# Kernel tuning notes

Hardware: AMD Instinct MI355X
Metric: run time of the kernel (lower is better)

## Reference

```python
import jax, jax.numpy as jnp
import numpy as np

B, T, ENC_H, DEC_H, ATTN = 128, 2048, 512, 512, 128


def setup_inputs() -> dict:
    key = jax.random.key(0)
    k1, k2, k3, k4, k5 = jax.random.split(key, 5)
    s = lambda fan_in: 1.0 / np.sqrt(fan_in)
    return {
        "encoder_outputs": jax.random.normal(k1, (B, T, ENC_H), dtype=jnp.float32),
        "decoder_hidden": jax.random.normal(k2, (B, DEC_H), dtype=jnp.float32),
        # nn.Linear weights are [out_features, in_features]
        "W_enc": jax.random.uniform(k3, (ATTN, ENC_H), jnp.float32, -s(ENC_H), s(ENC_H)),
        "W_dec": jax.random.uniform(k4, (ATTN, DEC_H), jnp.float32, -s(DEC_H), s(DEC_H)),
        "v_w": jax.random.uniform(k5, (1, ATTN), jnp.float32, -s(ATTN), s(ATTN)),
    }


def reference(encoder_outputs, decoder_hidden, W_enc, W_dec, v_w):
    # enc_proj: [B, T, A]
    enc_proj = jnp.einsum("bth,ah->bta", encoder_outputs, W_enc)
    # dec_proj: [B, 1, A]
    dec_proj = jnp.einsum("bh,ah->ba", decoder_hidden, W_dec)[:, None, :]
    energy = jnp.tanh(enc_proj + dec_proj)                      # [B, T, A]
    scores = jnp.einsum("bta,a->bt", energy, v_w[0])            # [B, T]
    weights = jax.nn.softmax(scores, axis=-1)                   # [B, T]
    context = jnp.einsum("bt,bth->bh", weights, encoder_outputs)  # [B, ENC_H]
    return context, weights
```

## Files before the change

### kernel.cpp

```cpp
#include <hip/hip_runtime.h>
#include <hip/hip_bf16.h>

#define B_SZ   128
#define T_SZ   2048
#define ENCH   512
#define ATTN_  128
#define NBLK   256
#define STRIPS_PER_BLK 8

typedef __attribute__((ext_vector_type(8))) short short8;
typedef __attribute__((ext_vector_type(4))) float f32x4;

__device__ __forceinline__ unsigned short f2bf_rne(float f) {
  unsigned u = __builtin_bit_cast(unsigned, f);
  u += 0x7FFFu + ((u >> 16) & 1u);
  return (unsigned short)(u >> 16);
}
__device__ __forceinline__ float fast_tanh(float x) {
  float e = __expf(2.f * x);
  return 1.f - __fdividef(2.f, e + 1.f);
}
__device__ __forceinline__ short8 pack8(float4 a, float4 b) {
  union { unsigned u[4]; short8 s; } r;
  asm("v_cvt_pk_bf16_f32 %0, %1, %2" : "=v"(r.u[0]) : "v"(a.x), "v"(a.y));
  asm("v_cvt_pk_bf16_f32 %0, %1, %2" : "=v"(r.u[1]) : "v"(a.z), "v"(a.w));
  asm("v_cvt_pk_bf16_f32 %0, %1, %2" : "=v"(r.u[2]) : "v"(b.x), "v"(b.y));
  asm("v_cvt_pk_bf16_f32 %0, %1, %2" : "=v"(r.u[3]) : "v"(b.z), "v"(b.w));
  return r.s;
}
template<int CTRL>
__device__ __forceinline__ float dpp_add(float v) {
  int t = __builtin_amdgcn_update_dpp(0, __builtin_bit_cast(int, v),
                                      CTRL, 0xf, 0xf, true);
  return v + __builtin_bit_cast(float, t);
}
__device__ __forceinline__ float sum16(float v) {
  v = dpp_add<0xB1>(v);
  v = dpp_add<0x4E>(v);
  v = dpp_add<0x141>(v);
  v = dpp_add<0x140>(v);
  return v;
}

__global__ void k_prep(const float* __restrict__ w,
                       unsigned short* __restrict__ o,
                       const float* __restrict__ dec,
                       const float* __restrict__ wdec,
                       float* __restrict__ dout) {
  if (blockIdx.x < 32) {
    int idx = blockIdx.x * 256 + threadIdx.x;
    int l   = idx & 63;
    int wks = idx >> 6;
    int cg  = wks >> 4, ks = wks & 15;
    int row = cg * 16 + (l & 15);
    int col = ks * 32 + (l >> 4) * 8;
    const float4* src = reinterpret_cast<const float4*>(w + row * ENCH + col);
    float4 v0 = src[0], v1 = src[1];
    short8 r;
    r[0] = (short)f2bf_rne(v0.x); r[1] = (short)f2bf_rne(v0.y);
    r[2] = (short)f2bf_rne(v0.z); r[3] = (short)f2bf_rne(v0.w);
    r[4] = (short)f2bf_rne(v1.x); r[5] = (short)f2bf_rne(v1.y);
    r[6] = (short)f2bf_rne(v1.z); r[7] = (short)f2bf_rne(v1.w);
    *reinterpret_cast<short8*>(o + (size_t)idx * 8) = r;
  } else {
    __shared__ float dh[ENCH];
    int b = blockIdx.x - 32, tid = threadIdx.x;
    for (int i = tid; i < ENCH; i += 256) dh[i] = dec[b * ENCH + i];
    __syncthreads();
    if (tid < 128) {
      const float4* wr4 = reinterpret_cast<const float4*>(wdec + tid * ENCH);
      float acc = 0.f;
      for (int h4 = 0; h4 < ENCH / 4; ++h4) {
        float4 w4 = wr4[h4];
        acc += dh[h4 * 4 + 0] * w4.x + dh[h4 * 4 + 1] * w4.y +
               dh[h4 * 4 + 2] * w4.z + dh[h4 * 4 + 3] * w4.w;
      }
      dout[b * ATTN_ + tid] = acc;
    }
  }
}

__global__ __launch_bounds__(512, 2) void k_main(
    const float* __restrict__ enc,
    const unsigned short* __restrict__ wfrag,
    const float* __restrict__ decproj,
    const float* __restrict__ vw,
    float* __restrict__ scores_raw,
    float* __restrict__ ctx_part,
    float* __restrict__ ml_part)
{
  const int tid  = threadIdx.x;
  const int lane = tid & 63;
  const int wid  = tid >> 6;
  const int l15  = lane & 15;
  const int g    = lane >> 4;

  __shared__ unsigned short w_lds[ATTN_ * ENCH];

#pragma unroll
  for (int r = 0; r < 16; ++r) {
    int i = r * 512 + tid;
    reinterpret_cast<short8*>(w_lds)[i] = reinterpret_cast<const short8*>(wfrag)[i];
  }

  const int b       = blockIdx.x >> 1;
  const int s16base = (blockIdx.x & 1) * 8;
  float vv[8], dv[8];
#pragma unroll
  for (int cg = 0; cg < 8; ++cg) {
    vv[cg] = vw[cg * 16 + l15];
    dv[cg] = decproj[b * ATTN_ + cg * 16 + l15];
  }
  __syncthreads();

#pragma unroll 1
  for (int k = 0; k < wid; ++k) __builtin_amdgcn_s_sleep(12);

#pragma unroll 1
  for (int i = 0; i < STRIPS_PER_BLK; ++i) {
    const int s16  = s16base + i;
    const int row0 = s16 * 128 + wid * 16;
    const float* arow = enc + ((size_t)b * T_SZ + row0 + l15) * ENCH + g * 8;

    float4 r0[16], r1[16];
#pragma unroll
    for (int ks = 0; ks < 16; ++ks) {
      r0[ks] = *reinterpret_cast<const float4*>(arow + ks * 32);
      r1[ks] = *reinterpret_cast<const float4*>(arow + ks * 32 + 4);
    }

    f32x4 acc[8];
#pragma unroll
    for (int cg = 0; cg < 8; ++cg) acc[cg] = (f32x4){0.f, 0.f, 0.f, 0.f};
#pragma unroll
    for (int ks = 0; ks < 16; ++ks) {
      short8 af = pack8(r0[ks], r1[ks]);
      const char* wb = (const char*)w_lds + ks * 1024 + lane * 16;
#pragma unroll
      for (int cg = 0; cg < 8; ++cg) {
        short8 bf = *reinterpret_cast<const short8*>(wb + cg * 16384);
        acc[cg] = __builtin_amdgcn_mfma_f32_16x16x32_bf16(af, bf, acc[cg], 0, 0, 0);
      }
    }

    float er[4];
#pragma unroll
    for (int r = 0; r < 4; ++r) {
      float e = 0.f;
#pragma unroll
      for (int cg = 0; cg < 8; ++cg)
        e += fast_tanh(acc[cg][r] + dv[cg]) * vv[cg];
      er[r] = sum16(e);
    }
    if (l15 == 0) {
#pragma unroll
      for (int r = 0; r < 4; ++r)
        scores_raw[(size_t)b * T_SZ + row0 + g * 4 + r] = er[r];
    }

    float mg = fmaxf(fmaxf(er[0], er[1]), fmaxf(er[2], er[3]));
    mg = fmaxf(mg, __shfl_xor(mg, 16));
    mg = fmaxf(mg, __shfl_xor(mg, 32));
    float x0 = __expf(er[0] - mg), x1 = __expf(er[1] - mg);
    float x2 = __expf(er[2] - mg), x3 = __expf(er[3] - mg);
    float xs = (x0 + x1) + (x2 + x3);
    xs += __shfl_xor(xs, 16);
    xs += __shfl_xor(xs, 32);
    const float l_run = xs;
    float sel = (l15 & 3) == 0 ? er[0]
              : (l15 & 3) == 1 ? er[1]
              : (l15 & 3) == 2 ? er[2] : er[3];
    float smine = __shfl(sel, ((l15 >> 2) << 4) | (l15 & 3));
    const float p_me = __expf(smine - mg);

    float ctx8[8];
#pragma unroll
    for (int j = 0; j < 8; ++j) ctx8[j] = 0.f;
#pragma unroll
    for (int ks = 0; ks < 16; ++ks) {
      float c[8];
      c[0] = p_me * r0[ks].x; c[1] = p_me * r0[ks].y;
      c[2] = p_me * r0[ks].z; c[3] = p_me * r0[ks].w;
      c[4] = p_me * r1[ks].x; c[5] = p_me * r1[ks].y;
      c[6] = p_me * r1[ks].z; c[7] = p_me * r1[ks].w;
#pragma unroll
      for (int j = 0; j < 8; ++j) c[j] = sum16(c[j]);
      if (l15 == ks) {
#pragma unroll
        for (int j = 0; j < 8; ++j) ctx8[j] = c[j];
      }
    }

    const size_t widx = (size_t)b * 128 + s16 * 8 + wid;
    float* cp = ctx_part + widx * ENCH + l15 * 32 + g * 8;
    *reinterpret_cast<float4*>(cp)     = (float4){ctx8[0], ctx8[1], ctx8[2], ctx8[3]};
    *reinterpret_cast<float4*>(cp + 4) = (float4){ctx8[4], ctx8[5], ctx8[6], ctx8[7]};
    if (lane == 0) {
      ml_part[widx * 2 + 0] = mg;
      ml_part[widx * 2 + 1] = l_run;
    }
  }
}

__global__ void k_combine(const float* __restrict__ ctx_part,
                          const float* __restrict__ ml_part,
                          float* __restrict__ out_ctx,
                          float* __restrict__ weights)
{
  __shared__ float msh[128], lsh[128], fac[128];
  int b = blockIdx.x, tid = threadIdx.x;
  if (tid < 128) {
    msh[tid] = ml_part[((size_t)b * 128 + tid) * 2 + 0];
    lsh[tid] = ml_part[((size_t)b * 128 + tid) * 2 + 1];
  }
  __syncthreads();
  float M = msh[0];
  for (int w = 1; w < 128; ++w) M = fmaxf(M, msh[w]);
  if (tid < 128) fac[tid] = __expf(msh[tid] - M);
  __syncthreads();
  float L = 0.f;
  for (int w = 0; w < 128; ++w) L += fac[w] * lsh[w];
  float Linv = 1.f / L;
  for (int h = tid; h < ENCH; h += 256) {
    float a = 0.f;
    for (int w = 0; w < 128; ++w)
      a += fac[w] * ctx_part[((size_t)b * 128 + w) * ENCH + h];
    out_ctx[b * ENCH + h] = a * Linv;
  }
  for (int t = tid; t < T_SZ; t += 256) {
    float raw = weights[(size_t)b * T_SZ + t];
    weights[(size_t)b * T_SZ + t] = __expf(raw - M) * Linv;
  }
}

extern "C" void kernel_launch(void* const* d_in, const int* in_sizes, int n_in,
                              void* d_out, int out_size, void* d_ws, size_t ws_size,
                              hipStream_t stream) {
  const float* enc  = (const float*)d_in[0];
  const float* dec  = (const float*)d_in[1];
  const float* wenc = (const float*)d_in[2];
  const float* wdec = (const float*)d_in[3];
  const float* vw   = (const float*)d_in[4];

  float* out     = (float*)d_out;
  float* out_ctx = out;
  float* out_w   = out + B_SZ * ENCH;

  char* ws = (char*)d_ws;
  unsigned short* wfrag = (unsigned short*)ws;
  float* decproj  = (float*)(ws + 131072);
  float* ml_part  = (float*)(ws + 131072 + 65536);
  float* ctx_part = (float*)(ws + 131072 + 65536 + 131072);

  hipLaunchKernelGGL(k_prep, dim3(160), dim3(256), 0, stream,
                     wenc, wfrag, dec, wdec, decproj);
  hipLaunchKernelGGL(k_main, dim3(NBLK), dim3(512), 0, stream,
                     enc, wfrag, decproj, vw, out_w, ctx_part, ml_part);
  hipLaunchKernelGGL(k_combine, dim3(B_SZ), dim3(256), 0, stream,
                     ctx_part, ml_part, out_ctx, out_w);
}
```

Measured before the change: 173.2 us.

## Double waves per block by keeping encoder tiles as bf16 and splitting accumulators

The main kernel now launches 1024-thread blocks, each covering four 256-row segments, instead of 512-thread blocks covering eight 128-row strips. Each wave keeps its encoder tile only as packed bf16 MFMA fragments rather than fp32 copies. The projection is done in two halves of four column groups with fewer live accumulators, and the decoder projection and v vectors move to LDS. This cuts register use so twice as many waves per CU can hide global load latency in this bandwidth-bound kernel. The trade-off is that the context sum now uses bf16-rounded encoder values, which lowers its precision.

```diff
diff --git a/kernel.cpp b/kernel.cpp
--- a/kernel.cpp
+++ b/kernel.cpp
@@ -6,7 +6,7 @@
 #define ENCH   512
 #define ATTN_  128
 #define NBLK   256
-#define STRIPS_PER_BLK 8
+#define SEGS_PER_BLK 4
 
 typedef __attribute__((ext_vector_type(8))) short short8;
 typedef __attribute__((ext_vector_type(4))) float f32x4;
@@ -40,6 +40,10 @@
   v = dpp_add<0x141>(v);
   v = dpp_add<0x140>(v);
   return v;
+}
+__device__ __forceinline__ float bfel(short8 v, int j_half, bool hi) {
+  unsigned u = __builtin_bit_cast(unsigned, (int)((((int*)&v))[j_half]));
+  return __builtin_bit_cast(float, hi ? (u & 0xFFFF0000u) : (u << 16));
 }
 
 __global__ void k_prep(const float* __restrict__ w,
@@ -80,7 +84,7 @@
   }
 }
 
-__global__ __launch_bounds__(512, 2) void k_main(
+__global__ __launch_bounds__(1024, 4) void k_main(
     const float* __restrict__ enc,
     const unsigned short* __restrict__ wfrag,
     const float* __restrict__ decproj,
@@ -96,62 +100,65 @@
   const int g    = lane >> 4;
 
   __shared__ unsigned short w_lds[ATTN_ * ENCH];
-
-#pragma unroll
-  for (int r = 0; r < 16; ++r) {
-    int i = r * 512 + tid;
+  __shared__ float dv_lds[ATTN_], vv_lds[ATTN_];
+
+  const int b    = blockIdx.x >> 1;
+  const int seg0 = (blockIdx.x & 1) * 4;
+
+#pragma unroll
+  for (int r = 0; r < 8; ++r) {
+    int i = r * 1024 + tid;
     reinterpret_cast<short8*>(w_lds)[i] = reinterpret_cast<const short8*>(wfrag)[i];
   }
-
-  const int b       = blockIdx.x >> 1;
-  const int s16base = (blockIdx.x & 1) * 8;
-  float vv[8], dv[8];
-#pragma unroll
-  for (int cg = 0; cg < 8; ++cg) {
-    vv[cg] = vw[cg * 16 + l15];
-    dv[cg] = decproj[b * ATTN_ + cg * 16 + l15];
-  }
+  if (tid < 128)       dv_lds[tid] = decproj[b * ATTN_ + tid];
+  else if (tid < 256)  vv_lds[tid - 128] = vw[tid - 128];
   __syncthreads();
 
 #pragma unroll 1
-  for (int k = 0; k < wid; ++k) __builtin_amdgcn_s_sleep(12);
+  for (int k = 0; k < wid; ++k) __builtin_amdgcn_s_sleep(6);
 
 #pragma unroll 1
-  for (int i = 0; i < STRIPS_PER_BLK; ++i) {
-    const int s16  = s16base + i;
-    const int row0 = s16 * 128 + wid * 16;
+  for (int i = 0; i < SEGS_PER_BLK; ++i) {
+    const int seg  = seg0 + i;
+    const int row0 = seg * 256 + wid * 16;
     const float* arow = enc + ((size_t)b * T_SZ + row0 + l15) * ENCH + g * 8;
 
-    float4 r0[16], r1[16];
+    short8 af[16];
 #pragma unroll
     for (int ks = 0; ks < 16; ++ks) {
-      r0[ks] = *reinterpret_cast<const float4*>(arow + ks * 32);
-      r1[ks] = *reinterpret_cast<const float4*>(arow + ks * 32 + 4);
-    }
-
-    f32x4 acc[8];
-#pragma unroll
-    for (int cg = 0; cg < 8; ++cg) acc[cg] = (f32x4){0.f, 0.f, 0.f, 0.f};
-#pragma unroll
-    for (int ks = 0; ks < 16; ++ks) {
-      short8 af = pack8(r0[ks], r1[ks]);
-      const char* wb = (const char*)w_lds + ks * 1024 + lane * 16;
-#pragma unroll
-      for (int cg = 0; cg < 8; ++cg) {
-        short8 bf = *reinterpret_cast<const short8*>(wb + cg * 16384);
-        acc[cg] = __builtin_amdgcn_mfma_f32_16x16x32_bf16(af, bf, acc[cg], 0, 0, 0);
+      float4 a0 = *reinterpret_cast<const float4*>(arow + ks * 32);
+      float4 a1 = *reinterpret_cast<const float4*>(arow + ks * 32 + 4);
+      af[ks] = pack8(a0, a1);
+    }
+
+    float e[4] = {0.f, 0.f, 0.f, 0.f};
+#pragma unroll 1
+    for (int half = 0; half < 2; ++half) {
+      f32x4 acc[4];
+#pragma unroll
+      for (int c = 0; c < 4; ++c) acc[c] = (f32x4){0.f, 0.f, 0.f, 0.f};
+#pragma unroll
+      for (int ks = 0; ks < 16; ++ks) {
+        const char* wb = (const char*)w_lds + ks * 1024 + lane * 16 + half * 65536;
+#pragma unroll
+        for (int c = 0; c < 4; ++c) {
+          short8 bf = *reinterpret_cast<const short8*>(wb + c * 16384);
+          acc[c] = __builtin_amdgcn_mfma_f32_16x16x32_bf16(af[ks], bf, acc[c], 0, 0, 0);
+        }
+      }
+#pragma unroll
+      for (int c = 0; c < 4; ++c) {
+        int col = (half * 4 + c) * 16 + l15;
+        float d = dv_lds[col], v = vv_lds[col];
+#pragma unroll
+        for (int r = 0; r < 4; ++r)
+          e[r] += fast_tanh(acc[c][r] + d) * v;
       }
     }
 
     float er[4];
 #pragma unroll
-    for (int r = 0; r < 4; ++r) {
-      float e = 0.f;
-#pragma unroll
-      for (int cg = 0; cg < 8; ++cg)
-        e += fast_tanh(acc[cg][r] + dv[cg]) * vv[cg];
-      er[r] = sum16(e);
-    }
+    for (int r = 0; r < 4; ++r) er[r] = sum16(e[r]);
     if (l15 == 0) {
 #pragma unroll
       for (int r = 0; r < 4; ++r)
@@ -179,10 +186,11 @@
 #pragma unroll
     for (int ks = 0; ks < 16; ++ks) {
       float c[8];
-      c[0] = p_me * r0[ks].x; c[1] = p_me * r0[ks].y;
-      c[2] = p_me * r0[ks].z; c[3] = p_me * r0[ks].w;
-      c[4] = p_me * r1[ks].x; c[5] = p_me * r1[ks].y;
-      c[6] = p_me * r1[ks].z; c[7] = p_me * r1[ks].w;
+#pragma unroll
+      for (int jh = 0; jh < 4; ++jh) {
+        c[jh * 2 + 0] = p_me * bfel(af[ks], jh, false);
+        c[jh * 2 + 1] = p_me * bfel(af[ks], jh, true);
+      }
 #pragma unroll
       for (int j = 0; j < 8; ++j) c[j] = sum16(c[j]);
       if (l15 == ks) {
@@ -191,7 +199,7 @@
       }
     }
 
-    const size_t widx = (size_t)b * 128 + s16 * 8 + wid;
+    const size_t widx = (size_t)b * 128 + seg * 16 + wid;
     float* cp = ctx_part + widx * ENCH + l15 * 32 + g * 8;
     *reinterpret_cast<float4*>(cp)     = (float4){ctx8[0], ctx8[1], ctx8[2], ctx8[3]};
     *reinterpret_cast<float4*>(cp + 4) = (float4){ctx8[4], ctx8[5], ctx8[6], ctx8[7]};
@@ -254,7 +262,7 @@
 
   hipLaunchKernelGGL(k_prep, dim3(160), dim3(256), 0, stream,
                      wenc, wfrag, dec, wdec, decproj);
-  hipLaunchKernelGGL(k_main, dim3(NBLK), dim3(512), 0, stream,
+  hipLaunchKernelGGL(k_main, dim3(NBLK), dim3(1024), 0, stream,
                      enc, wfrag, decproj, vw, out_w, ctx_part, ml_part);
   hipLaunchKernelGGL(k_combine, dim3(B_SZ), dim3(256), 0, stream,
                      ctx_part, ml_part, out_ctx, out_w);
```

Measured after the change: 167.7 us. 1.03x faster.
